# Kernel optimization log

Hardware: AMD Instinct MI355X
Metric: run time of the kernel (lower is better)

Reference implementation:

```python
import jax, jax.numpy as jnp
import numpy as np

B, N, COUT, CIN, H, W = 16, 4, 256, 256, 64, 64


def setup_inputs() -> dict:
    key = jax.random.key(0)
    k1, k2, k3, k4 = jax.random.split(key, 4)
    x = jax.random.normal(k1, (B, CIN, H, W), jnp.float32)
    alphas = jax.random.uniform(k2, (B, N), jnp.float32)          # routing weights (lambdas)
    angles = jax.random.normal(k3, (B, N), jnp.float32) * 0.5     # thetas, mixed signs
    # kaiming_normal_(mode='fan_out', relu): std = sqrt(2 / (Cout * k * k))
    std = np.sqrt(2.0 / (COUT * 9)).astype(np.float32)
    weight = jax.random.normal(k4, (N, COUT, CIN, 3, 3), jnp.float32) * std
    return {"x": x, "alphas": alphas, "angles": angles, "weight": weight}


def _rot_mats(thetas):
    """thetas: [M] -> rotation matrices [M, 9, 9] (row, col), matching torch builder."""
    xc = jnp.cos(thetas)
    ys = jnp.sin(thetas)
    a = xc - ys
    b = xc * ys
    c = xc + ys
    z = jnp.zeros_like(xc)
    o = jnp.ones_like(xc)

    def mat(rows):
        # rows: list of 9 lists of 9 [M]-arrays -> [M, 9, 9]
        return jnp.stack([jnp.stack(r, axis=-1) for r in rows], axis=-2)

    pos = mat([
        [a, 1 - a, z, z, z, z, z, z, z],
        [z, xc - b, b, z, 1 - c + b, ys - b, z, z, z],
        [z, z, a, z, z, 1 - a, z, z, z],
        [b, ys - b, z, xc - b, 1 - c + b, z, z, z, z],
        [z, z, z, z, o, z, z, z, z],
        [z, z, z, z, 1 - c + b, xc - b, z, ys - b, b],
        [z, z, z, 1 - a, z, z, a, z, z],
        [z, z, z, ys - b, 1 - c + b, z, b, xc - b, z],
        [z, z, z, z, z, z, z, 1 - a, a],
    ])
    neg = mat([
        [c, z, z, 1 - c, z, z, z, z, z],
        [-b, xc + b, z, b - ys, 1 - a - b, z, z, z, z],
        [z, 1 - c, c, z, z, z, z, z, z],
        [z, z, z, xc + b, 1 - a - b, z, -b, b - ys, z],
        [z, z, z, z, o, z, z, z, z],
        [z, b - ys, -b, z, 1 - a - b, xc + b, z, z, z],
        [z, z, z, z, z, z, c, 1 - c, z],
        [z, z, z, z, 1 - a - b, b - ys, z, xc + b, -b],
        [z, z, z, z, z, 1 - c, z, z, c],
    ])
    m = (thetas >= 0).astype(thetas.dtype)[:, None, None]
    return m * pos + (1 - m) * neg


def reference(x, alphas, angles, weight):
    bsz, Cin, h, w = x.shape
    n, Cout = weight.shape[0], weight.shape[1]
    # [bsz, n, 9, 9] rotation matrices scaled by routing lambdas
    rm = _rot_mats(angles.reshape(-1)).reshape(bsz, n, 9, 9)
    rm = rm * alphas[:, :, None, None]
    # weights [n, Cout, Cin, 3, 3] -> [n, 9, Cout*Cin]
    Wf = weight.transpose(0, 3, 4, 1, 2).reshape(n, 9, Cout * Cin)
    # mix over kernel_number n and source tap q -> per-sample rotated kernels
    rw = jnp.einsum('bnpq,nqm->bpm', rm, Wf)          # [bsz, 9, Cout*Cin]
    rw = rw.reshape(bsz, 3, 3, Cout, Cin).transpose(0, 3, 4, 1, 2)
    rw = rw.reshape(bsz * Cout, Cin, 3, 3)
    # per-sample conv via grouped conv on flattened batch
    xr = x.reshape(1, bsz * Cin, h, w)
    out = jax.lax.conv_general_dilated(
        xr, rw, window_strides=(1, 1), padding=((1, 1), (1, 1)),
        dimension_numbers=('NCHW', 'OIHW', 'NCHW'), feature_group_count=bsz)
    return out.reshape(bsz, Cout, out.shape[2], out.shape[3])
```

## Files before the change

kernel.cpp:

```cpp
#include <hip/hip_runtime.h>
#include <hip/hip_bf16.h>

#define B_    16
#define N_    4
#define COUT  256
#define CIN   256
#define H_    64
#define W_    64
#define K_TOT (CIN * 9)
#define HW    (H_ * W_)
#define NKT   72
#define PAD   66
#define PLANE (PAD * PAD)

typedef __attribute__((ext_vector_type(8))) short short8;
typedef __attribute__((ext_vector_type(4))) float f32x4;
typedef unsigned short ushort_t;

static __device__ __forceinline__ ushort_t f2bf(float f) {
    __hip_bfloat16 h = __float2bfloat16(f);
    return *reinterpret_cast<ushort_t*>(&h);
}

typedef __attribute__((address_space(3))) unsigned int lds_u32;
typedef __attribute__((address_space(1))) const unsigned int glb_u32;
static __device__ __forceinline__ void gl_lds16(const ushort_t* g, ushort_t* l) {
    __builtin_amdgcn_global_load_lds((glb_u32*)g, (lds_u32*)l, 16, 0, 0);
}

#define BARRIER() asm volatile("s_barrier" ::: "memory")
#define VMCNTN(N) asm volatile("s_waitcnt vmcnt(" #N ")" ::: "memory")

__global__ __launch_bounds__(256)
void build_rw_kernel(const float* __restrict__ weight,
                     const float* __restrict__ alphas,
                     const float* __restrict__ angles,
                     ushort_t* __restrict__ rw) {
    __shared__ float rms[N_ * 81];
    int tid = threadIdx.x;
    int b = blockIdx.y;

    if (tid < N_) {
        int i = b * N_ + tid;
        float th = angles[i], al = alphas[i];
        float xc = cosf(th), ys = sinf(th);
        float a = xc - ys, bb = xc * ys, c = xc + ys;
        float r[81];
#pragma unroll
        for (int j = 0; j < 81; ++j) r[j] = 0.f;
        if (th >= 0.f) {
            r[0] = a;          r[1] = 1.f - a;
            r[10] = xc - bb;   r[11] = bb;       r[13] = 1.f - c + bb; r[14] = ys - bb;
            r[20] = a;         r[23] = 1.f - a;
            r[27] = bb;        r[28] = ys - bb;  r[30] = xc - bb;      r[31] = 1.f - c + bb;
            r[40] = 1.f;
            r[49] = 1.f - c + bb; r[50] = xc - bb; r[52] = ys - bb;    r[53] = bb;
            r[57] = 1.f - a;   r[60] = a;
            r[66] = ys - bb;   r[67] = 1.f - c + bb; r[69] = bb;       r[70] = xc - bb;
            r[79] = 1.f - a;   r[80] = a;
        } else {
            r[0] = c;          r[3] = 1.f - c;
            r[9] = -bb;        r[10] = xc + bb;  r[12] = bb - ys;      r[13] = 1.f - a - bb;
            r[19] = 1.f - c;   r[20] = c;
            r[30] = xc + bb;   r[31] = 1.f - a - bb; r[33] = -bb;      r[34] = bb - ys;
            r[40] = 1.f;
            r[46] = bb - ys;   r[47] = -bb;      r[49] = 1.f - a - bb; r[50] = xc + bb;
            r[60] = c;         r[61] = 1.f - c;
            r[67] = 1.f - a - bb; r[68] = bb - ys; r[70] = xc + bb;    r[71] = -bb;
            r[77] = 1.f - c;   r[80] = c;
        }
#pragma unroll
        for (int j = 0; j < 81; ++j) rms[tid * 81 + j] = r[j] * al;
    }
    __syncthreads();

    int idx = blockIdx.x * 256 + tid;
    int cout = idx >> 8, cin = idx & 255;

    float wv[N_][9];
#pragma unroll
    for (int n = 0; n < N_; ++n)
#pragma unroll
        for (int q = 0; q < 9; ++q)
            wv[n][q] = weight[(size_t)(n * (COUT * CIN) + idx) * 9 + q];

    ushort_t* dst = rw + (size_t)(b * COUT + cout) * K_TOT + cin;
#pragma unroll
    for (int p = 0; p < 9; ++p) {
        float s = 0.f;
#pragma unroll
        for (int n = 0; n < N_; ++n)
#pragma unroll
            for (int q = 0; q < 9; ++q)
                s += rms[n * 81 + p * 9 + q] * wv[n][q];
        dst[p * 256] = f2bf(s);
    }
}

__global__ __launch_bounds__(256)
void nhwc_kernel(const float* __restrict__ x, ushort_t* __restrict__ xt) {
    int y    = blockIdx.x;
    int cb32 = blockIdx.y;
    int b    = blockIdx.z;
    __shared__ ushort_t tileT[64][40];
    int t = threadIdx.x;

    ushort_t* plane = xt + (size_t)(b * 4 + (cb32 >> 1)) * PLANE * 64 + (cb32 & 1) * 32;
    const int4 z = {0, 0, 0, 0};

    int ci = t & 31, seg = t >> 5;
    const float* src = x + ((size_t)(b * CIN + cb32 * 32 + ci) * HW + y * 64 + seg * 8);
    float4 f0 = ((const float4*)src)[0];
    float4 f1 = ((const float4*)src)[1];
#pragma unroll
    for (int q = 0; q < 4; ++q) tileT[seg * 8 + q][ci]     = f2bf(((float*)&f0)[q]);
#pragma unroll
    for (int q = 0; q < 4; ++q) tileT[seg * 8 + 4 + q][ci] = f2bf(((float*)&f1)[q]);

    if (t < 8) {
        int col = (t >> 2) ? 65 : 0;
        int sg  = t & 3;
        *(int4*)(plane + ((size_t)(y + 1) * PAD + col) * 64 + sg * 8) = z;
    }
    if (y == 0) {
        for (int u = t; u < 528; u += 256) {
            int row = (u >= 264) ? 65 : 0;
            int v = (u >= 264) ? u - 264 : u;
            int px = v >> 2, sg = v & 3;
            *(int4*)(plane + ((size_t)row * PAD + px) * 64 + sg * 8) = z;
        }
    }
    __syncthreads();

    int px = t >> 2, cseg = t & 3;
    ushort_t* dst = plane + ((size_t)(y + 1) * PAD + px + 1) * 64 + cseg * 8;
    *(int4*)dst = *(const int4*)&tileT[px][cseg * 8];
}

__global__ __launch_bounds__(512, 1)
void conv_kernel(const ushort_t* __restrict__ xt,
                 const ushort_t* __restrict__ rw,
                 float* __restrict__ out) {
    int bid0 = blockIdx.x;
    int bid = (bid0 & 7) * 32 + (bid0 >> 3);
    int b     = bid >> 4;
    int ptile = bid & 15;
    int y0 = ptile * 4;
    int tid = threadIdx.x;
    int lane = tid & 63, wid = tid >> 6;
    int wm = wid >> 2, wn = wid & 3;
    int rA = lane & 15, kseg = lane >> 4;

    __shared__ __align__(16) ushort_t As[3][8192];
    __shared__ __align__(16) ushort_t Bs[3][8192];
    ushort_t* AsB = &As[0][0];
    ushort_t* BsB = &Bs[0][0];

    f32x4 acc[8][4] = {};

    const ushort_t* rwb = rw + (size_t)b * COUT * K_TOT;
    const ushort_t* xtb = xt + ((size_t)b * 4 * PLANE + (size_t)y0 * PAD) * 64;

    int asrc[2], bsrc[2], uDst[2];
#pragma unroll
    for (int i = 0; i < 2; ++i) {
        int u = i * 512 + tid;
        int l = u >> 3, s = u & 7;
        int c = s ^ (l & 7);
        int row = 2 * l + (c >> 2);
        asrc[i] = row * K_TOT + (c & 3) * 8;
        bsrc[i] = ((row >> 6) * PAD + (row & 63)) * 64 + (c & 3) * 8;
        uDst[i] = u * 8;
    }
    const int slotR = (kseg + 4 * (rA & 1)) ^ ((rA >> 1) & 7);
    const int aRd = (wm * 64 + (rA >> 1)) * 64 + slotR * 8;
    const int bRd = (wn * 32 + (rA >> 1)) * 64 + slotR * 8;

#define STAGE_AB(KT, Q)                                                        \
    {                                                                          \
        int p_ = (KT) >> 3, sub_ = (KT) & 7;                                   \
        int ako = p_ * 256 + sub_ * 32;                                        \
        gl_lds16(rwb + asrc[0] + ako, AsB + (Q) * 8192 + uDst[0]);             \
        gl_lds16(rwb + asrc[1] + ako, AsB + (Q) * 8192 + uDst[1]);             \
        int ph_ = p_ / 3, pw_ = p_ - 3 * ph_;                                  \
        const ushort_t* sb_ = xtb + (size_t)((sub_ >> 1) * PLANE + ph_ * PAD + pw_) * 64 \
                              + (sub_ & 1) * 32;                               \
        gl_lds16(sb_ + bsrc[0], BsB + (Q) * 8192 + uDst[0]);                   \
        gl_lds16(sb_ + bsrc[1], BsB + (Q) * 8192 + uDst[1]);                   \
    }

#define READ_FRAGS(Q, AF, BF)                                                  \
    _Pragma("unroll")                                                          \
    for (int mi = 0; mi < 8; ++mi)                                             \
        AF[mi] = *(const short8*)(AsB + (Q) * 8192 + aRd + mi * 512);          \
    _Pragma("unroll")                                                          \
    for (int ni = 0; ni < 4; ++ni)                                             \
        BF[ni] = *(const short8*)(BsB + (Q) * 8192 + bRd + ni * 512);

#define TILE_BODY(KT, QN, QS, AFC, BFC, AFN, BFN)                              \
    {                                                                          \
        if ((KT) + 1 < NKT) { READ_FRAGS(QN, AFN, BFN); }                      \
        if ((KT) + 2 < NKT) { STAGE_AB((KT) + 2, QS); }                        \
        __builtin_amdgcn_s_setprio(1);                                         \
        _Pragma("unroll")                                                      \
        for (int mi = 0; mi < 8; ++mi)                                         \
            _Pragma("unroll")                                                  \
            for (int ni = 0; ni < 4; ++ni)                                     \
                acc[mi][ni] = __builtin_amdgcn_mfma_f32_16x16x32_bf16(         \
                    AFC[mi], BFC[ni], acc[mi][ni], 0, 0, 0);                   \
        __builtin_amdgcn_s_setprio(0);                                         \
        VMCNTN(0);                                                             \
        BARRIER();                                                             \
    }

    STAGE_AB(0, 0);
    STAGE_AB(1, 1);
    VMCNTN(0);
    BARRIER();

    short8 afA[8], bfA[4], afB[8], bfB[4];
    READ_FRAGS(0, afA, bfA);

    int qc = 0;
    for (int kt = 0; kt < NKT; kt += 2) {
        int qn = qc + 1; if (qn >= 3) qn -= 3;
        int qs = qc + 2; if (qs >= 3) qs -= 3;
        TILE_BODY(kt, qn, qs, afA, bfA, afB, bfB);
        int qn2 = qs;
        int qs2 = qc;
        TILE_BODY(kt + 1, qn2, qs2, afB, bfB, afA, bfA);
        qc = qs;
    }
#undef TILE_BODY
#undef READ_FRAGS
#undef STAGE_AB

    int row0 = (lane >> 4) * 4;
    int col  = lane & 15;
    float* outb = out + (size_t)b * COUT * HW + ptile * 256;
#pragma unroll
    for (int am = 0; am < 8; ++am)
#pragma unroll
        for (int an = 0; an < 4; ++an)
#pragma unroll
            for (int rr = 0; rr < 4; ++rr) {
                int m = wm * 128 + am * 16 + row0 + rr;
                int n = wn * 64 + an * 16 + col;
                outb[(size_t)m * HW + n] = acc[am][an][rr];
            }
}

extern "C" void kernel_launch(void* const* d_in, const int* in_sizes, int n_in,
                              void* d_out, int out_size, void* d_ws, size_t ws_size,
                              hipStream_t stream) {
    const float* x      = (const float*)d_in[0];
    const float* alphas = (const float*)d_in[1];
    const float* angles = (const float*)d_in[2];
    const float* weight = (const float*)d_in[3];
    float* out = (float*)d_out;

    ushort_t* rw = (ushort_t*)d_ws;
    ushort_t* xt = (ushort_t*)((char*)d_ws + (size_t)B_ * COUT * K_TOT * 2);

    build_rw_kernel<<<dim3(COUT * CIN / 256, B_), 256, 0, stream>>>(weight, alphas, angles, rw);
    nhwc_kernel<<<dim3(64, 8, B_), 256, 0, stream>>>(x, xt);
    conv_kernel<<<256, 512, 0, stream>>>(xt, rw, out);
}
```

Measured before the change: 111.5 us.

## Switch conv GEMM to 64-wide K tiles with double-buffered quarter-staged loads

```diff
diff --git a/kernel.cpp b/kernel.cpp
--- a/kernel.cpp
+++ b/kernel.cpp
@@ -9,7 +9,7 @@
 #define W_    64
 #define K_TOT (CIN * 9)
 #define HW    (H_ * W_)
-#define NKT   72
+#define NKT   36
 #define PAD   66
 #define PLANE (PAD * PAD)
 
@@ -151,8 +151,8 @@
     int wm = wid >> 2, wn = wid & 3;
     int rA = lane & 15, kseg = lane >> 4;
 
-    __shared__ __align__(16) ushort_t As[3][8192];
-    __shared__ __align__(16) ushort_t Bs[3][8192];
+    __shared__ __align__(16) ushort_t As[2][16384];
+    __shared__ __align__(16) ushort_t Bs[2][16384];
     ushort_t* AsB = &As[0][0];
     ushort_t* BsB = &Bs[0][0];
 
@@ -161,79 +161,99 @@
     const ushort_t* rwb = rw + (size_t)b * COUT * K_TOT;
     const ushort_t* xtb = xt + ((size_t)b * 4 * PLANE + (size_t)y0 * PAD) * 64;
 
-    int asrc[2], bsrc[2], uDst[2];
-#pragma unroll
-    for (int i = 0; i < 2; ++i) {
-        int u = i * 512 + tid;
-        int l = u >> 3, s = u & 7;
-        int c = s ^ (l & 7);
-        int row = 2 * l + (c >> 2);
-        asrc[i] = row * K_TOT + (c & 3) * 8;
-        bsrc[i] = ((row >> 6) * PAD + (row & 63)) * 64 + (c & 3) * 8;
-        uDst[i] = u * 8;
-    }
-    const int slotR = (kseg + 4 * (rA & 1)) ^ ((rA >> 1) & 7);
-    const int aRd = (wm * 64 + (rA >> 1)) * 64 + slotR * 8;
-    const int bRd = (wn * 32 + (rA >> 1)) * 64 + slotR * 8;
-
-#define STAGE_AB(KT, Q)                                                        \
+    const int rq = tid >> 3;
+    const int cs = ((tid & 7) ^ (rq & 7)) * 8;
+    const int dl = tid * 8;
+
+#define RSLOT(KH) ((((KH) << 2) | kseg) ^ (rA & 7)) * 8
+
+#define STAGE_A2(KT, Q, Q0, Q1)                                                \
     {                                                                          \
-        int p_ = (KT) >> 3, sub_ = (KT) & 7;                                   \
-        int ako = p_ * 256 + sub_ * 32;                                        \
-        gl_lds16(rwb + asrc[0] + ako, AsB + (Q) * 8192 + uDst[0]);             \
-        gl_lds16(rwb + asrc[1] + ako, AsB + (Q) * 8192 + uDst[1]);             \
+        int p_ = (KT) >> 2, c4_ = (KT) & 3;                                    \
+        int ako = p_ * 256 + c4_ * 64;                                         \
+        gl_lds16(rwb + (size_t)((Q0) * 64 + rq) * K_TOT + cs + ako,            \
+                 AsB + (Q) * 16384 + (Q0) * 4096 + dl);                        \
+        gl_lds16(rwb + (size_t)((Q1) * 64 + rq) * K_TOT + cs + ako,            \
+                 AsB + (Q) * 16384 + (Q1) * 4096 + dl);                        \
+    }
+
+#define STAGE_B2(KT, Q, Q0, Q1)                                                \
+    {                                                                          \
+        int p_ = (KT) >> 2, c4_ = (KT) & 3;                                    \
         int ph_ = p_ / 3, pw_ = p_ - 3 * ph_;                                  \
-        const ushort_t* sb_ = xtb + (size_t)((sub_ >> 1) * PLANE + ph_ * PAD + pw_) * 64 \
-                              + (sub_ & 1) * 32;                               \
-        gl_lds16(sb_ + bsrc[0], BsB + (Q) * 8192 + uDst[0]);                   \
-        gl_lds16(sb_ + bsrc[1], BsB + (Q) * 8192 + uDst[1]);                   \
-    }
-
-#define READ_FRAGS(Q, AF, BF)                                                  \
+        const ushort_t* sb_ = xtb + (size_t)(c4_ * PLANE + ph_ * PAD + pw_) * 64; \
+        gl_lds16(sb_ + (size_t)((Q0) * PAD + rq) * 64 + cs,                    \
+                 BsB + (Q) * 16384 + (Q0) * 4096 + dl);                        \
+        gl_lds16(sb_ + (size_t)((Q1) * PAD + rq) * 64 + cs,                    \
+                 BsB + (Q) * 16384 + (Q1) * 4096 + dl);                        \
+    }
+
+#define READ_AF(Q, MH, KH)                                                     \
     _Pragma("unroll")                                                          \
-    for (int mi = 0; mi < 8; ++mi)                                             \
-        AF[mi] = *(const short8*)(AsB + (Q) * 8192 + aRd + mi * 512);          \
+    for (int mi = 0; mi < 4; ++mi) {                                           \
+        int row = wm * 128 + (MH) * 64 + mi * 16 + rA;                         \
+        af[mi] = *(const short8*)(AsB + (Q) * 16384 + row * 64 + RSLOT(KH));   \
+    }
+
+#define READ_BF(Q, KH)                                                         \
     _Pragma("unroll")                                                          \
-    for (int ni = 0; ni < 4; ++ni)                                             \
-        BF[ni] = *(const short8*)(BsB + (Q) * 8192 + bRd + ni * 512);
-
-#define TILE_BODY(KT, QN, QS, AFC, BFC, AFN, BFN)                              \
-    {                                                                          \
-        if ((KT) + 1 < NKT) { READ_FRAGS(QN, AFN, BFN); }                      \
-        if ((KT) + 2 < NKT) { STAGE_AB((KT) + 2, QS); }                        \
-        __builtin_amdgcn_s_setprio(1);                                         \
+    for (int ni = 0; ni < 4; ++ni) {                                           \
+        int row = wn * 64 + ni * 16 + rA;                                      \
+        bf[ni] = *(const short8*)(BsB + (Q) * 16384 + row * 64 + RSLOT(KH));   \
+    }
+
+#define DO_MFMA(MH)                                                            \
+    __builtin_amdgcn_s_setprio(1);                                             \
+    _Pragma("unroll")                                                          \
+    for (int mi = 0; mi < 4; ++mi)                                             \
         _Pragma("unroll")                                                      \
-        for (int mi = 0; mi < 8; ++mi)                                         \
-            _Pragma("unroll")                                                  \
-            for (int ni = 0; ni < 4; ++ni)                                     \
-                acc[mi][ni] = __builtin_amdgcn_mfma_f32_16x16x32_bf16(         \
-                    AFC[mi], BFC[ni], acc[mi][ni], 0, 0, 0);                   \
-        __builtin_amdgcn_s_setprio(0);                                         \
-        VMCNTN(0);                                                             \
-        BARRIER();                                                             \
-    }
-
-    STAGE_AB(0, 0);
-    STAGE_AB(1, 1);
-    VMCNTN(0);
+        for (int ni = 0; ni < 4; ++ni)                                         \
+            acc[(MH) * 4 + mi][ni] = __builtin_amdgcn_mfma_f32_16x16x32_bf16(  \
+                af[mi], bf[ni], acc[(MH) * 4 + mi][ni], 0, 0, 0);              \
+    __builtin_amdgcn_s_setprio(0);
+
+    STAGE_B2(0, 0, 0, 1);
+    STAGE_B2(0, 0, 2, 3);
+    STAGE_A2(0, 0, 0, 2);
+    STAGE_A2(0, 0, 1, 3);
+    VMCNTN(2);
     BARRIER();
 
-    short8 afA[8], bfA[4], afB[8], bfB[4];
-    READ_FRAGS(0, afA, bfA);
-
-    int qc = 0;
-    for (int kt = 0; kt < NKT; kt += 2) {
-        int qn = qc + 1; if (qn >= 3) qn -= 3;
-        int qs = qc + 2; if (qs >= 3) qs -= 3;
-        TILE_BODY(kt, qn, qs, afA, bfA, afB, bfB);
-        int qn2 = qs;
-        int qs2 = qc;
-        TILE_BODY(kt + 1, qn2, qs2, afB, bfB, afA, bfA);
-        qc = qs;
-    }
-#undef TILE_BODY
-#undef READ_FRAGS
-#undef STAGE_AB
+    short8 af[4], bf[4];
+    for (int kt = 0; kt < NKT; ++kt) {
+        int q = kt & 1, qn = q ^ 1;
+        bool more = (kt + 1 < NKT);
+        READ_AF(q, 0, 0);
+        READ_BF(q, 0);
+        if (more) STAGE_B2(kt + 1, qn, 0, 1);
+        BARRIER();
+        DO_MFMA(0);
+        if (more) { VMCNTN(2); } else { VMCNTN(0); }
+        BARRIER();
+        READ_AF(q, 1, 0);
+        if (more) STAGE_B2(kt + 1, qn, 2, 3);
+        BARRIER();
+        DO_MFMA(1);
+        BARRIER();
+        READ_AF(q, 0, 1);
+        READ_BF(q, 1);
+        if (more) STAGE_A2(kt + 1, qn, 0, 2);
+        BARRIER();
+        DO_MFMA(0);
+        BARRIER();
+        READ_AF(q, 1, 1);
+        if (more) STAGE_A2(kt + 1, qn, 1, 3);
+        BARRIER();
+        DO_MFMA(1);
+        VMCNTN(2);
+        BARRIER();
+    }
+#undef STAGE_A2
+#undef STAGE_B2
+#undef READ_AF
+#undef READ_BF
+#undef DO_MFMA
+#undef RSLOT
 
     int row0 = (lane >> 4) * 4;
     int col  = lane & 15;
```

After: 107.5 us (median of 2 runs). 1.04x faster.
